# Kernel tuning notes

Measured on AMD Instinct MI355X. Metric: run time of the kernel, lower is better.

The kernel has to match this reference:

```python
import jax, jax.numpy as jnp
import numpy as np

B = 8192
D_IN = 512
UNITS = 512


def setup_inputs() -> dict:
    key = jax.random.key(0)
    ks = jax.random.split(key, 9)
    sx = 1.0 / np.sqrt(D_IN)
    sh = 1.0 / np.sqrt(UNITS)
    return {
        "input_x": jax.random.normal(ks[0], (B, D_IN), jnp.float32),
        "input_h": jax.random.normal(ks[1], (B, UNITS), jnp.float32),
        "attention_score": jax.random.uniform(ks[2], (B, 1), jnp.float32),
        "Wx_r": jax.random.normal(ks[3], (D_IN, UNITS), jnp.float32) * sx,
        "b_r": jnp.zeros((UNITS,), jnp.float32),
        "Wh_r": jax.random.normal(ks[4], (UNITS, UNITS), jnp.float32) * sh,
        "Wx_u": jax.random.normal(ks[5], (D_IN, UNITS), jnp.float32) * sx,
        "b_u": jnp.zeros((UNITS,), jnp.float32),
        "Wh_u": jax.random.normal(ks[6], (UNITS, UNITS), jnp.float32) * sh,
        "Wx_h": jax.random.normal(ks[7], (D_IN, UNITS), jnp.float32) * sx,
        "b_h": jnp.zeros((UNITS,), jnp.float32),
        "Wh_h": jax.random.normal(ks[8], (UNITS, UNITS), jnp.float32) * sh,
    }


def reference(input_x, input_h, attention_score,
              Wx_r, b_r, Wh_r,
              Wx_u, b_u, Wh_u,
              Wx_h, b_h, Wh_h):
    # reset gate: sigmoid(Dense_b(x) + Dense(h))
    r = jax.nn.sigmoid(input_x @ Wx_r + b_r + input_h @ Wh_r)
    # update gate: sigmoid(Dense_b(x) + Dense(h))
    u = jax.nn.sigmoid(input_x @ Wx_u + b_u + input_h @ Wh_u)
    # candidate: tanh(Dense_b(x) + r * Dense(h))
    cal_h = jnp.tanh(input_x @ Wx_h + b_h + r * (input_h @ Wh_h))
    # attention-modulated update and interpolation
    u_att = attention_score * u
    h = (1.0 - u_att) * input_h + u_att * cal_h
    return h
```

## Files before the change

kernel.cpp:

```cpp
#include <hip/hip_runtime.h>
#include <hip/hip_bf16.h>

typedef __bf16 bf16x8 __attribute__((ext_vector_type(8)));
typedef float f32x4 __attribute__((ext_vector_type(4)));
typedef unsigned short us8 __attribute__((ext_vector_type(8)));

#define MFMA16 __builtin_amdgcn_mfma_f32_16x16x32_bf16

__device__ __forceinline__ unsigned short f2bf(float f) {
    unsigned int u = __float_as_uint(f);
    u += 0x7fffu + ((u >> 16) & 1u);
    return (unsigned short)(u >> 16);
}

__device__ __forceinline__ void gload_lds16(const void* g, void* l) {
    __builtin_amdgcn_global_load_lds(
        (const __attribute__((address_space(1))) unsigned int*)g,
        (__attribute__((address_space(3))) unsigned int*)l, 16, 0, 0);
}

__global__ void cvt_all_kernel(const float* __restrict__ x, const float* __restrict__ h,
                               unsigned short* __restrict__ AP,
                               const float* __restrict__ W0, const float* __restrict__ W1,
                               const float* __restrict__ W2, const float* __restrict__ W3,
                               const float* __restrict__ W4, const float* __restrict__ W5,
                               unsigned short* __restrict__ WP) {
    if (blockIdx.x < 4096) {
        int c = blockIdx.x * 256 + threadIdx.x;
        int ih = c >> 19;
        const float* src = ih ? h : x;
        int c2 = c & 524287;
        int mb = c2 >> 10, kb = (c2 >> 6) & 15, lane = c2 & 63;
        int r = lane & 15, ko = lane >> 4;
        const float* p = src + (size_t)(mb * 16 + r) * 512 + kb * 32 + ko * 8;
        float4 v0 = *(const float4*)p;
        float4 v1 = *(const float4*)(p + 4);
        us8 o = { f2bf(v0.x), f2bf(v0.y), f2bf(v0.z), f2bf(v0.w),
                  f2bf(v1.x), f2bf(v1.y), f2bf(v1.z), f2bf(v1.w) };
        *((us8*)AP + ((size_t)(mb * 32 + kb + ih * 16) << 6) + lane) = o;
    } else {
        int c = (blockIdx.x - 4096) * 256 + threadIdx.x;
        int s = c >> 16, c2 = c & 65535;
        int frag = c2 >> 6, lane = c2 & 63;
        int nb = frag >> 5, kbp = frag & 31;
        const float* Wsrc;
        int kb;
        if (kbp < 16) { kb = kbp;      Wsrc = (s == 0) ? W0 : (s == 1) ? W2 : W4; }
        else          { kb = kbp - 16; Wsrc = (s == 0) ? W1 : (s == 1) ? W3 : W5; }
        int cc = lane & 15, ko = lane >> 4;
        int kbase = kb * 32 + ko * 8;
        us8 o;
#pragma unroll
        for (int e = 0; e < 8; ++e)
            o[e] = f2bf(Wsrc[(size_t)(kbase + e) * 512 + nb * 16 + cc]);
        *((us8*)WP + c) = o;
    }
}

__global__ __launch_bounds__(512, 2) void augru_mm(
    const unsigned short* __restrict__ AP_,
    const unsigned short* __restrict__ WP_,
    const float* __restrict__ b_r, const float* __restrict__ b_u, const float* __restrict__ b_h,
    const float* __restrict__ att, const float* __restrict__ h32,
    float* __restrict__ out) {
    __shared__ unsigned char sA[65536];
    const unsigned char* APb = (const unsigned char*)AP_;
    const unsigned char* WPb = (const unsigned char*)WP_;

    const int t0 = threadIdx.x, wv = t0 >> 6, lane = t0 & 63;
    const int laneoff = lane * 16;

    const int bid = blockIdx.x;
    const int Wid = (bid & 7) * 32 + (bid >> 3);
    const int mblk = Wid >> 3, nblk = Wid & 7;
    const int wr = wv >> 1, wc = wv & 1;

    f32x4 accR[4][2] = {}, accU[4][2] = {}, accXH[4][2] = {}, accHH[4][2] = {};

    const unsigned char* gA[4];
    unsigned dsA[4];
#pragma unroll
    for (int mf = 0; mf < 4; ++mf) {
        int mb = mblk * 16 + wr * 4 + mf;
        gA[mf] = APb + ((size_t)(mb * 32) << 10) + laneoff;
        dsA[mf] = (unsigned)(wv * 8192 + mf * 1024);
    }
    const unsigned char* gB[3][2];
#pragma unroll
    for (int s = 0; s < 3; ++s)
#pragma unroll
        for (int nf = 0; nf < 2; ++nf)
            gB[s][nf] = WPb + (size_t)s * 1048576 +
                        ((size_t)((nblk * 4 + wc * 2 + nf) * 32) << 10) + laneoff;

    bf16x8 a[4], b0[3][2], b1[3][2];

#pragma unroll
    for (int mf = 0; mf < 4; ++mf)
        gload_lds16(gA[mf], (unsigned char*)sA + dsA[mf]);
    asm volatile("" ::: "memory");
#pragma unroll
    for (int s = 0; s < 3; ++s)
#pragma unroll
        for (int nf = 0; nf < 2; ++nf)
            b0[s][nf] = *(const bf16x8*)(gB[s][nf]);
    asm volatile("" ::: "memory");
#pragma unroll
    for (int mf = 0; mf < 4; ++mf)
        gload_lds16(gA[mf] + 1024, (unsigned char*)sA + dsA[mf] + 4096);
    asm volatile("" ::: "memory");
#pragma unroll
    for (int s = 0; s < 3; ++s)
#pragma unroll
        for (int nf = 0; nf < 2; ++nf)
            b1[s][nf] = *(const bf16x8*)(gB[s][nf] + 1024);

#define BODY(T, P, BREG, ACCC, VMC, PF) { \
    asm volatile("s_waitcnt vmcnt(" VMC ")" ::: "memory"); \
    _Pragma("unroll") for (int mf = 0; mf < 4; ++mf) \
        a[mf] = *(const bf16x8*)((const unsigned char*)sA + dsA[mf] + (P) * 4096 + laneoff); \
    asm volatile("s_waitcnt lgkmcnt(0)" ::: "memory"); \
    if (PF) { _Pragma("unroll") for (int mf = 0; mf < 4; ++mf) \
        gload_lds16(gA[mf] + ((size_t)((T) + 2) << 10), \
                    (unsigned char*)sA + dsA[mf] + (P) * 4096); } \
    __builtin_amdgcn_s_setprio(1); \
    _Pragma("unroll") for (int mf = 0; mf < 4; ++mf) \
      _Pragma("unroll") for (int nf = 0; nf < 2; ++nf) { \
        accR[mf][nf] = MFMA16(a[mf], BREG[0][nf], accR[mf][nf], 0, 0, 0); \
        accU[mf][nf] = MFMA16(a[mf], BREG[1][nf], accU[mf][nf], 0, 0, 0); \
        ACCC[mf][nf] = MFMA16(a[mf], BREG[2][nf], ACCC[mf][nf], 0, 0, 0); } \
    __builtin_amdgcn_s_setprio(0); \
    if (PF) { _Pragma("unroll") for (int s = 0; s < 3; ++s) \
      _Pragma("unroll") for (int nf = 0; nf < 2; ++nf) \
        BREG[s][nf] = *(const bf16x8*)(gB[s][nf] + ((size_t)((T) + 2) << 10)); } \
}

#pragma unroll 1
    for (int i = 0; i < 8; ++i) {
        const int te = 2 * i;
        BODY(te,     0, b0, accXH, "10", true)
        BODY(te + 1, 1, b1, accXH, "10", true)
    }
#pragma unroll 1
    for (int i = 8; i < 15; ++i) {
        const int te = 2 * i;
        BODY(te,     0, b0, accHH, "10", true)
        BODY(te + 1, 1, b1, accHH, "10", true)
    }
    BODY(30, 0, b0, accHH, "10", false)
    BODY(31, 1, b1, accHH, "0",  false)

    const int lr = lane & 15, lg = lane >> 4;
#pragma unroll
    for (int nf = 0; nf < 2; ++nf) {
        const int col = nblk * 64 + wc * 32 + nf * 16 + lr;
        const float br = b_r[col], bu = b_u[col], bh = b_h[col];
#pragma unroll
        for (int mf = 0; mf < 4; ++mf) {
            const int rowb = mblk * 256 + wr * 64 + mf * 16 + lg * 4;
#pragma unroll
            for (int q = 0; q < 4; ++q) {
                const int row = rowb + q;
                float r = 1.f / (1.f + __expf(-(accR[mf][nf][q] + br)));
                float u = 1.f / (1.f + __expf(-(accU[mf][nf][q] + bu)));
                float ph = accXH[mf][nf][q] + bh + r * accHH[mf][nf][q];
                ph = fminf(fmaxf(ph, -15.f), 15.f);
                float e = __expf(2.f * ph);
                float cal = (e - 1.f) / (e + 1.f);
                float hv = h32[(size_t)row * 512 + col];
                float ua = att[row] * u;
                out[(size_t)row * 512 + col] = fmaf(ua, cal - hv, hv);
            }
        }
    }
#undef BODY
}

extern "C" void kernel_launch(void* const* d_in, const int* in_sizes, int n_in,
                              void* d_out, int out_size, void* d_ws, size_t ws_size,
                              hipStream_t stream) {
    const float* x    = (const float*)d_in[0];
    const float* h    = (const float*)d_in[1];
    const float* att  = (const float*)d_in[2];
    const float* Wx_r = (const float*)d_in[3];
    const float* b_r  = (const float*)d_in[4];
    const float* Wh_r = (const float*)d_in[5];
    const float* Wx_u = (const float*)d_in[6];
    const float* b_u  = (const float*)d_in[7];
    const float* Wh_u = (const float*)d_in[8];
    const float* Wx_h = (const float*)d_in[9];
    const float* b_h  = (const float*)d_in[10];
    const float* Wh_h = (const float*)d_in[11];
    float* out = (float*)d_out;

    unsigned short* AP = (unsigned short*)d_ws;
    unsigned short* WP = AP + 8388608;

    cvt_all_kernel<<<4864, 256, 0, stream>>>(x, h, AP,
        Wx_r, Wh_r, Wx_u, Wh_u, Wx_h, Wh_h, WP);
    augru_mm<<<256, 512, 0, stream>>>(AP, WP, b_r, b_u, b_h, att, h, out);
}
```

Before: 48.72 us.

## Load A fragments directly from global into registers, dropping LDS staging

```diff
diff --git a/kernel.cpp b/kernel.cpp
--- a/kernel.cpp
+++ b/kernel.cpp
@@ -11,12 +11,6 @@
     unsigned int u = __float_as_uint(f);
     u += 0x7fffu + ((u >> 16) & 1u);
     return (unsigned short)(u >> 16);
-}
-
-__device__ __forceinline__ void gload_lds16(const void* g, void* l) {
-    __builtin_amdgcn_global_load_lds(
-        (const __attribute__((address_space(1))) unsigned int*)g,
-        (__attribute__((address_space(3))) unsigned int*)l, 16, 0, 0);
 }
 
 __global__ void cvt_all_kernel(const float* __restrict__ x, const float* __restrict__ h,
@@ -63,9 +57,8 @@
     const float* __restrict__ b_r, const float* __restrict__ b_u, const float* __restrict__ b_h,
     const float* __restrict__ att, const float* __restrict__ h32,
     float* __restrict__ out) {
-    __shared__ unsigned char sA[65536];
-    const unsigned char* APb = (const unsigned char*)AP_;
-    const unsigned char* WPb = (const unsigned char*)WP_;
+    const unsigned char* __restrict__ APb = (const unsigned char*)AP_;
+    const unsigned char* __restrict__ WPb = (const unsigned char*)WP_;
 
     const int t0 = threadIdx.x, wv = t0 >> 6, lane = t0 & 63;
     const int laneoff = lane * 16;
@@ -77,78 +70,74 @@
 
     f32x4 accR[4][2] = {}, accU[4][2] = {}, accXH[4][2] = {}, accHH[4][2] = {};
 
-    const unsigned char* gA[4];
-    unsigned dsA[4];
+    const unsigned char* __restrict__ pA[4];
+    const unsigned char* __restrict__ pB[3][2];
 #pragma unroll
-    for (int mf = 0; mf < 4; ++mf) {
-        int mb = mblk * 16 + wr * 4 + mf;
-        gA[mf] = APb + ((size_t)(mb * 32) << 10) + laneoff;
-        dsA[mf] = (unsigned)(wv * 8192 + mf * 1024);
-    }
-    const unsigned char* gB[3][2];
+    for (int mf = 0; mf < 4; ++mf)
+        pA[mf] = APb + ((size_t)((mblk * 16 + wr * 4 + mf) * 32) << 10) + laneoff;
 #pragma unroll
     for (int s = 0; s < 3; ++s)
 #pragma unroll
         for (int nf = 0; nf < 2; ++nf)
-            gB[s][nf] = WPb + (size_t)s * 1048576 +
+            pB[s][nf] = WPb + (size_t)s * 1048576 +
                         ((size_t)((nblk * 4 + wc * 2 + nf) * 32) << 10) + laneoff;
 
-    bf16x8 a[4], b0[3][2], b1[3][2];
-
+    bf16x8 aN[4], bN[3][2];
 #pragma unroll
-    for (int mf = 0; mf < 4; ++mf)
-        gload_lds16(gA[mf], (unsigned char*)sA + dsA[mf]);
-    asm volatile("" ::: "memory");
+    for (int mf = 0; mf < 4; ++mf) aN[mf] = *(const bf16x8*)(pA[mf]);
 #pragma unroll
     for (int s = 0; s < 3; ++s)
 #pragma unroll
-        for (int nf = 0; nf < 2; ++nf)
-            b0[s][nf] = *(const bf16x8*)(gB[s][nf]);
-    asm volatile("" ::: "memory");
-#pragma unroll
-    for (int mf = 0; mf < 4; ++mf)
-        gload_lds16(gA[mf] + 1024, (unsigned char*)sA + dsA[mf] + 4096);
-    asm volatile("" ::: "memory");
-#pragma unroll
-    for (int s = 0; s < 3; ++s)
-#pragma unroll
-        for (int nf = 0; nf < 2; ++nf)
-            b1[s][nf] = *(const bf16x8*)(gB[s][nf] + 1024);
+        for (int nf = 0; nf < 2; ++nf) bN[s][nf] = *(const bf16x8*)(pB[s][nf]);
 
-#define BODY(T, P, BREG, ACCC, VMC, PF) { \
-    asm volatile("s_waitcnt vmcnt(" VMC ")" ::: "memory"); \
+#define ROTATE_LOAD(T1) { \
     _Pragma("unroll") for (int mf = 0; mf < 4; ++mf) \
-        a[mf] = *(const bf16x8*)((const unsigned char*)sA + dsA[mf] + (P) * 4096 + laneoff); \
-    asm volatile("s_waitcnt lgkmcnt(0)" ::: "memory"); \
-    if (PF) { _Pragma("unroll") for (int mf = 0; mf < 4; ++mf) \
-        gload_lds16(gA[mf] + ((size_t)((T) + 2) << 10), \
-                    (unsigned char*)sA + dsA[mf] + (P) * 4096); } \
-    __builtin_amdgcn_s_setprio(1); \
+        aN[mf] = *(const bf16x8*)(pA[mf] + ((size_t)(T1) << 10)); \
+    _Pragma("unroll") for (int s = 0; s < 3; ++s) \
+      _Pragma("unroll") for (int nf = 0; nf < 2; ++nf) \
+        bN[s][nf] = *(const bf16x8*)(pB[s][nf] + ((size_t)(T1) << 10)); }
+
+#define MFMAS(ACCC) { \
     _Pragma("unroll") for (int mf = 0; mf < 4; ++mf) \
       _Pragma("unroll") for (int nf = 0; nf < 2; ++nf) { \
-        accR[mf][nf] = MFMA16(a[mf], BREG[0][nf], accR[mf][nf], 0, 0, 0); \
-        accU[mf][nf] = MFMA16(a[mf], BREG[1][nf], accU[mf][nf], 0, 0, 0); \
-        ACCC[mf][nf] = MFMA16(a[mf], BREG[2][nf], ACCC[mf][nf], 0, 0, 0); } \
-    __builtin_amdgcn_s_setprio(0); \
-    if (PF) { _Pragma("unroll") for (int s = 0; s < 3; ++s) \
-      _Pragma("unroll") for (int nf = 0; nf < 2; ++nf) \
-        BREG[s][nf] = *(const bf16x8*)(gB[s][nf] + ((size_t)((T) + 2) << 10)); } \
-}
+        accR[mf][nf] = MFMA16(aC[mf], bC[0][nf], accR[mf][nf], 0, 0, 0); \
+        accU[mf][nf] = MFMA16(aC[mf], bC[1][nf], accU[mf][nf], 0, 0, 0); \
+        ACCC[mf][nf] = MFMA16(aC[mf], bC[2][nf], ACCC[mf][nf], 0, 0, 0); } }
 
-#pragma unroll 1
-    for (int i = 0; i < 8; ++i) {
-        const int te = 2 * i;
-        BODY(te,     0, b0, accXH, "10", true)
-        BODY(te + 1, 1, b1, accXH, "10", true)
+#pragma unroll 2
+    for (int T = 0; T < 16; ++T) {
+        bf16x8 aC[4], bC[3][2];
+#pragma unroll
+        for (int mf = 0; mf < 4; ++mf) aC[mf] = aN[mf];
+#pragma unroll
+        for (int s = 0; s < 3; ++s)
+#pragma unroll
+            for (int nf = 0; nf < 2; ++nf) bC[s][nf] = bN[s][nf];
+        ROTATE_LOAD(T + 1)
+        MFMAS(accXH)
     }
-#pragma unroll 1
-    for (int i = 8; i < 15; ++i) {
-        const int te = 2 * i;
-        BODY(te,     0, b0, accHH, "10", true)
-        BODY(te + 1, 1, b1, accHH, "10", true)
+#pragma unroll 2
+    for (int T = 16; T < 31; ++T) {
+        bf16x8 aC[4], bC[3][2];
+#pragma unroll
+        for (int mf = 0; mf < 4; ++mf) aC[mf] = aN[mf];
+#pragma unroll
+        for (int s = 0; s < 3; ++s)
+#pragma unroll
+            for (int nf = 0; nf < 2; ++nf) bC[s][nf] = bN[s][nf];
+        ROTATE_LOAD(T + 1)
+        MFMAS(accHH)
     }
-    BODY(30, 0, b0, accHH, "10", false)
-    BODY(31, 1, b1, accHH, "0",  false)
+    {
+        bf16x8 aC[4], bC[3][2];
+#pragma unroll
+        for (int mf = 0; mf < 4; ++mf) aC[mf] = aN[mf];
+#pragma unroll
+        for (int s = 0; s < 3; ++s)
+#pragma unroll
+            for (int nf = 0; nf < 2; ++nf) bC[s][nf] = bN[s][nf];
+        MFMAS(accHH)
+    }
 
     const int lr = lane & 15, lg = lane >> 4;
 #pragma unroll
@@ -173,7 +162,8 @@
             }
         }
     }
-#undef BODY
+#undef ROTATE_LOAD
+#undef MFMAS
 }
 
 extern "C" void kernel_launch(void* const* d_in, const int* in_sizes, int n_in,
```

New measurement: 54.07 us. 1.11x slower.
